# Performance work log

Measured on AMD Instinct MI355X. Metric: run time of the kernel, lower is better.

## Reference

```python
import jax, jax.numpy as jnp
import numpy as np

N = 50000   # nodes
E = 500000  # edges
B = 50      # graphs
H, D = 4, 64
NEG = 0.2   # leaky_relu slope in GATv2


def setup_inputs() -> dict:
    key = jax.random.key(0)
    ks = iter(jax.random.split(key, 40))
    rn = lambda shape, s=0.1: jax.random.normal(next(ks), shape, jnp.float32) * s
    inp = {
        'x': rn((N, 8), 1.0),
        'edge_index': jax.random.randint(next(ks), (2, E), 0, N, jnp.int64),
        'edge_attr': rn((E, 1), 1.0),
        'batch': jnp.sort(jax.random.randint(next(ks), (N,), 0, B, jnp.int64)),
        'enc_w': rn((8, 64)), 'enc_b': rn((64,)),
        'g1_wl': rn((64, 256)), 'g1_bl': rn((256,)),
        'g1_wr': rn((64, 256)), 'g1_br': rn((256,)),
        'g1_we': rn((1, 256)), 'g1_att': rn((H, D)), 'g1_bias': rn((256,)),
        'g2_wl': rn((256, 256)), 'g2_bl': rn((256,)),
        'g2_wr': rn((256, 256)), 'g2_br': rn((256,)),
        'g2_we': rn((1, 256)), 'g2_att': rn((H, D)), 'g2_bias': rn((256,)),
        'p1_w': rn((256, 128)), 'p1_b': rn((128,)),
        'ln_g': jnp.ones((128,), jnp.float32), 'ln_b': jnp.zeros((128,), jnp.float32),
        'p2_w': rn((128, 64)), 'p2_b': rn((64,)),
        'hc_w': rn((64, 1)), 'hc_b': rn((1,)),
        'hf_w': rn((64, 9)), 'hf_b': rn((9,)),
    }
    return inp


def gatv2(x, src, dst, ea, wl, bl, wr, br, we, att, bias):
    # x: [N, Fin]; src/dst: [E']; ea: [E',1]
    xl = (x @ wl + bl).reshape(N, H, D)  # source transform (lin_l)
    xr = (x @ wr + br).reshape(N, H, D)  # target transform (lin_r)
    e = (ea @ we).reshape(-1, H, D)      # edge embedding
    m = jax.nn.leaky_relu(xl[src] + xr[dst] + e, NEG)      # [E',H,D]
    logits = jnp.einsum('ehd,hd->eh', m, att)              # [E',H]
    # segment softmax over incoming edges of each target node
    lmax = jax.ops.segment_max(logits, dst, num_segments=N)
    lmax = jnp.where(jnp.isfinite(lmax), lmax, 0.0)
    ex = jnp.exp(logits - lmax[dst])
    den = jax.ops.segment_sum(ex, dst, num_segments=N)
    alpha = ex / den[dst]                                  # every node has a self-loop -> den > 0
    agg = jax.ops.segment_sum(xl[src] * alpha[:, :, None], dst, num_segments=N)
    return agg.reshape(N, H * D) + bias


def reference(x, edge_index, edge_attr, batch,
              enc_w, enc_b,
              g1_wl, g1_bl, g1_wr, g1_br, g1_we, g1_att, g1_bias,
              g2_wl, g2_bl, g2_wr, g2_br, g2_we, g2_att, g2_bias,
              p1_w, p1_b, ln_g, ln_b, p2_w, p2_b,
              hc_w, hc_b, hf_w, hf_b):
    # add self-loops once (PyG GATv2Conv default, edge_attr fill_value='mean')
    loop = jnp.arange(N, dtype=edge_index.dtype)
    src = jnp.concatenate([edge_index[0], loop])
    dst = jnp.concatenate([edge_index[1], loop])
    ea = jnp.concatenate([edge_attr,
                          jnp.broadcast_to(edge_attr.mean(0, keepdims=True), (N, 1))])

    h = jax.nn.relu(x @ enc_w + enc_b)
    h = jax.nn.relu(gatv2(h, src, dst, ea, g1_wl, g1_bl, g1_wr, g1_br, g1_we, g1_att, g1_bias))
    h = jax.nn.relu(gatv2(h, src, dst, ea, g2_wl, g2_bl, g2_wr, g2_br, g2_we, g2_att, g2_bias))

    # global mean pool over graphs
    sums = jax.ops.segment_sum(h, batch, num_segments=B)
    cnts = jax.ops.segment_sum(jnp.ones((N, 1), h.dtype), batch, num_segments=B)
    pooled = sums / jnp.maximum(cnts, 1.0)

    # post MLP: Linear -> LayerNorm -> ReLU -> (Dropout, eval=identity) -> Linear -> ReLU
    t = pooled @ p1_w + p1_b
    mu = t.mean(-1, keepdims=True)
    var = ((t - mu) ** 2).mean(-1, keepdims=True)
    t = (t - mu) / jnp.sqrt(var + 1e-5) * ln_g + ln_b
    t = jax.nn.relu(t)
    z = jax.nn.relu(t @ p2_w + p2_b)

    logit_cooling = (z @ hc_w + hc_b)[:, 0]
    logit_fatigue = z @ hf_w + hf_b
    return logit_cooling, logit_fatigue, z
```

## Files before the change

### kernel.cpp

```cpp
#include <hip/hip_runtime.h>
#include <hip/hip_bf16.h>

#define NN 50000
#define NE 500000
#define EP (NE + NN)
#define NB 50
#define NEG 0.2f
#define NBKT 196
#define CAP 3584
#define CHUNK 2048
#define NBLK1 ((EP + CHUNK - 1) / CHUNK)
#define NTILES 1563
#define GEMM_GX 392

#define ENC_BLKS 12500
#define MEAN_BLKS 256
#define WCONV_BLKS 640
#define ZERO_BLKS 51
#define SETUP_GRID (ENC_BLKS + MEAN_BLKS + WCONV_BLKS + 1 + ZERO_BLKS)

typedef __attribute__((ext_vector_type(8))) short short8;
typedef __attribute__((ext_vector_type(4))) float f32x4;

__device__ __forceinline__ ushort f2bf(float f) {
  unsigned u = __float_as_uint(f);
  unsigned r = (u + 0x7FFFu + ((u >> 16) & 1u)) >> 16;
  return (ushort)r;
}
__device__ __forceinline__ float bf2f(ushort b) {
  return __uint_as_float(((unsigned)b) << 16);
}

__device__ __forceinline__ float exp2s(float x) {
  float r;
  asm("v_exp_f32 %0, %1\ns_nop 0" : "=v"(r) : "v"(x));
  return r;
}

__device__ __forceinline__ float row_reduce16(float x) {
  x += __int_as_float(__builtin_amdgcn_mov_dpp(__float_as_int(x), 0xB1, 0xF, 0xF, true));
  x += __int_as_float(__builtin_amdgcn_mov_dpp(__float_as_int(x), 0x4E, 0xF, 0xF, true));
  x += __int_as_float(__builtin_amdgcn_mov_dpp(__float_as_int(x), 0x124, 0xF, 0xF, true));
  x += __int_as_float(__builtin_amdgcn_mov_dpp(__float_as_int(x), 0x128, 0xF, 0xF, true));
  return x;
}

__global__ __launch_bounds__(256) void setup_kernel(
    const float* __restrict__ x, const float* __restrict__ enc_w,
    const float* __restrict__ enc_b, ushort* __restrict__ h0,
    const float* __restrict__ ea, float* __restrict__ partials,
    const float* __restrict__ g1_wl, const float* __restrict__ g1_wr,
    const float* __restrict__ g2_wl, const float* __restrict__ g2_wr,
    ushort* __restrict__ w1l, ushort* __restrict__ w1r,
    ushort* __restrict__ w2l, ushort* __restrict__ w2r,
    const float* __restrict__ att1, const float* __restrict__ att2,
    float* __restrict__ a06_1, float* __restrict__ a04_1,
    float* __restrict__ a06_2, float* __restrict__ a04_2,
    int* __restrict__ gcursor, float* __restrict__ zero_region) {
  __shared__ float sw[4];
  int b = blockIdx.x, t = threadIdx.x;
  if (b < ENC_BLKS) {
    int i = b * 256 + t;
    int n = i >> 6, j = i & 63;
    float acc = enc_b[j];
#pragma unroll
    for (int k = 0; k < 8; k++) acc += x[n * 8 + k] * enc_w[k * 64 + j];
    h0[i] = f2bf(fmaxf(acc, 0.f));
    return;
  }
  b -= ENC_BLKS;
  if (b < MEAN_BLKS) {
    int idx = b * 256 + t;
    float v = 0.f;
    for (int i = idx; i < NE; i += 65536) v += ea[i];
    for (int off = 1; off < 64; off <<= 1) v += __shfl_xor(v, off, 64);
    if ((t & 63) == 0) sw[t >> 6] = v;
    __syncthreads();
    if (t == 0) partials[b] = sw[0] + sw[1] + sw[2] + sw[3];
    return;
  }
  b -= MEAN_BLKS;
  if (b < WCONV_BLKS) {
    if (b < 128) {
      int sec = b >> 6;
      const float* W = sec ? g1_wr : g1_wl;
      ushort* Wt = sec ? w1r : w1l;
      int i = (b & 63) * 256 + t;
      int n = i >> 6, k = i & 63;
      Wt[i] = f2bf(W[(size_t)k * 256 + n]);
    } else {
      int bb = b - 128;
      int sec = bb >> 8;
      const float* W = sec ? g2_wr : g2_wl;
      ushort* Wt = sec ? w2r : w2l;
      int i = (bb & 255) * 256 + t;
      int n = i >> 8, k = i & 255;
      Wt[i] = f2bf(W[(size_t)k * 256 + n]);
    }
    return;
  }
  b -= WCONV_BLKS;
  if (b == 0) {
    const float L2E = 1.44269504f;
    float v1 = att1[t], v2 = att2[t];
    a06_1[t] = 0.6f * L2E * v1;
    a04_1[t] = 0.4f * L2E * v1;
    a06_2[t] = 0.6f * L2E * v2;
    a04_2[t] = 0.4f * L2E * v2;
    if (t < NBKT) gcursor[t] = t * CAP;
    return;
  }
  b -= 1;
  {
    int i = b * 256 + t;
    if (i < NB * 256 + NB) zero_region[i] = 0.f;
  }
}

__global__ __launch_bounds__(256) void bucket_kernel(const int* __restrict__ ei,
                                                     const float* __restrict__ ea,
                                                     const float* __restrict__ partials,
                                                     int* __restrict__ gcursor,
                                                     int2* __restrict__ bucketed) {
  __shared__ int hist[NBKT];
  __shared__ int lbase[NBKT];
  __shared__ float smean[4];
  int t = threadIdx.x;
  int e0 = blockIdx.x * CHUNK;
  float pv = partials[t];
  for (int off = 1; off < 64; off <<= 1) pv += __shfl_xor(pv, off, 64);
  if ((t & 63) == 0) smean[t >> 6] = pv;
  for (int i = t; i < NBKT; i += 256) hist[i] = 0;
  __syncthreads();
  float mean = (smean[0] + smean[1] + smean[2] + smean[3]) * (1.0f / NE);
  int packed[8], eab[8], bkt[8];
#pragma unroll
  for (int j = 0; j < 8; j++) {
    int e = e0 + j * 256 + t;
    bool valid = e < EP;
    int src, dst;
    float v;
    if (e < NE) {
      src = ei[e];
      dst = ei[NE + e];
      v = ea[e];
    } else {
      int n = valid ? (e - NE) : 0;
      src = dst = n;
      v = mean;
    }
    bkt[j] = valid ? (dst >> 8) : -1;
    packed[j] = src | ((dst & 255) << 16);
    eab[j] = __float_as_int(v);
    if (valid) atomicAdd(&hist[dst >> 8], 1);
  }
  __syncthreads();
  for (int i = t; i < NBKT; i += 256)
    lbase[i] = hist[i] ? atomicAdd(&gcursor[i], hist[i]) : 0;
  __syncthreads();
#pragma unroll
  for (int j = 0; j < 8; j++) {
    if (bkt[j] >= 0) {
      int pos = atomicAdd(&lbase[bkt[j]], 1);
      pos = min(pos, (bkt[j] + 1) * CAP - 1);
      bucketed[pos] = make_int2(packed[j], eab[j]);
    }
  }
}

__global__ __launch_bounds__(256) void bucket_sort_kernel(const int* __restrict__ gcursor,
                                                          const int2* __restrict__ bucketed,
                                                          int2* __restrict__ sedge,
                                                          int* __restrict__ offsets,
                                                          int* __restrict__ counts) {
  __shared__ int2 stage[CAP];
  __shared__ int hist[256], scn[256], cur[256];
  int b = blockIdx.x, t = threadIdx.x;
  int base = b * CAP;
  int nb = min(gcursor[b] - base, CAP - 16);
  hist[t] = 0;
  for (int i = t; i < nb; i += 256) stage[i] = bucketed[base + i];
  __syncthreads();
  if (t < 16) {
    int2 pv = make_int2((stage[0].x & 0xFFFF) << 9, stage[0].y);
    sedge[base + nb + t] = pv;
  }
  for (int i = t; i < nb; i += 256) atomicAdd(&hist[(stage[i].x >> 16) & 255], 1);
  __syncthreads();
  int v = hist[t];
  scn[t] = v;
  __syncthreads();
  for (int off = 1; off < 256; off <<= 1) {
    int add = (t >= off) ? scn[t - off] : 0;
    __syncthreads();
    scn[t] += add;
    __syncthreads();
  }
  int excl = scn[t] - v;
  cur[t] = excl;
  __syncthreads();
  for (int i = t; i < nb; i += 256) {
    int dl = (stage[i].x >> 16) & 255;
    int p = atomicAdd(&cur[dl], 1);
    sedge[base + p] = make_int2((stage[i].x & 0xFFFF) << 9, stage[i].y);
  }
  int d = b * 256 + t;
  if (d < NN) {
    offsets[d] = base + excl;
    counts[d] = v;
  }
}

template <int K>
__global__ __launch_bounds__(256) void dual_linear_pb(const ushort* __restrict__ A,
                                                      const ushort* __restrict__ Wl,
                                                      const ushort* __restrict__ Wr,
                                                      const float* __restrict__ bl,
                                                      const float* __restrict__ br,
                                                      ushort* __restrict__ xl,
                                                      ushort* __restrict__ xr) {
  __shared__ ushort lt[32][272];
  int wave = threadIdx.x >> 6, lane = threadIdx.x & 63;
  int lr = lane & 15;
  int kb = (lane >> 4) * 8;
  const ushort* W = blockIdx.y ? Wr : Wl;
  const float* bias = blockIdx.y ? br : bl;
  ushort* O = blockIdx.y ? xr : xl;
  const int c0 = wave * 64;
  const ushort* pb = W + (size_t)(c0 + lr) * K + kb;
  int tid = threadIdx.x;
  int cb = (tid & 31) * 8;

  for (int t = blockIdx.x; t < NTILES; t += GEMM_GX) {
    int r = t * 32;
    int ra0 = min(r + lr, NN - 1);
    int ra1 = min(r + 16 + lr, NN - 1);
    const ushort* pa0 = A + (size_t)ra0 * K + kb;
    const ushort* pa1 = A + (size_t)ra1 * K + kb;
    f32x4 acc[2][4];
#pragma unroll
    for (int fr = 0; fr < 2; fr++)
#pragma unroll
      for (int fc = 0; fc < 4; fc++) acc[fr][fc] = (f32x4){0.f, 0.f, 0.f, 0.f};
#pragma unroll
    for (int kc = 0; kc < K; kc += 64) {
      short8 a00 = *(const short8*)(pa0 + kc);
      short8 a01 = *(const short8*)(pa0 + kc + 32);
      short8 a10 = *(const short8*)(pa1 + kc);
      short8 a11 = *(const short8*)(pa1 + kc + 32);
      short8 b0[4], b1[4];
#pragma unroll
      for (int fc = 0; fc < 4; fc++) {
        b0[fc] = *(const short8*)(pb + (size_t)fc * 16 * K + kc);
        b1[fc] = *(const short8*)(pb + (size_t)fc * 16 * K + kc + 32);
      }
#pragma unroll
      for (int fc = 0; fc < 4; fc++) {
        acc[0][fc] = __builtin_amdgcn_mfma_f32_16x16x32_bf16(a00, b0[fc], acc[0][fc], 0, 0, 0);
        acc[1][fc] = __builtin_amdgcn_mfma_f32_16x16x32_bf16(a10, b0[fc], acc[1][fc], 0, 0, 0);
      }
#pragma unroll
      for (int fc = 0; fc < 4; fc++) {
        acc[0][fc] = __builtin_amdgcn_mfma_f32_16x16x32_bf16(a01, b1[fc], acc[0][fc], 0, 0, 0);
        acc[1][fc] = __builtin_amdgcn_mfma_f32_16x16x32_bf16(a11, b1[fc], acc[1][fc], 0, 0, 0);
      }
    }
#pragma unroll
    for (int fc = 0; fc < 4; fc++) {
      int c = c0 + fc * 16 + lr;
      float bv = bias[c];
#pragma unroll
      for (int fr = 0; fr < 2; fr++) {
#pragma unroll
        for (int j = 0; j < 4; j++) {
          int row = fr * 16 + (lane >> 4) * 4 + j;
          int cs = c ^ (((row >> 2) & 3) << 4);
          lt[row][cs] = f2bf(acc[fr][fc][j] + bv);
        }
      }
    }
    __syncthreads();
#pragma unroll
    for (int it = 0; it < 4; it++) {
      int rl = (tid >> 5) + it * 8;
      int row = r + rl;
      if (row < NN) {
        int cs = cb ^ (((rl >> 2) & 3) << 4);
        short8 v = *(const short8*)&lt[rl][cs];
        *(short8*)(O + (size_t)row * 256 + cb) = v;
      }
    }
    __syncthreads();
  }
}

__global__ __launch_bounds__(256) void gat_fused_kernel(const int* __restrict__ offsets,
                                                        const int* __restrict__ counts,
                                                        const int2* __restrict__ sedge,
                                                        const ushort* __restrict__ xl,
                                                        const ushort* __restrict__ xr,
                                                        const float* __restrict__ we,
                                                        const float* __restrict__ a06p,
                                                        const float* __restrict__ a04p,
                                                        const float* __restrict__ bias,
                                                        ushort* __restrict__ hb) {
  int w = threadIdx.x >> 6, lane = threadIdx.x & 63;
  int d = blockIdx.x * 4 + w;
  if (d >= NN) return;
  int off = offsets[d], cnt = counts[d];
  const int c4 = lane * 4;
  ushort4 xru = *(const ushort4*)(xr + (size_t)d * 256 + c4);
  const float4 xr4 = {bf2f(xru.x), bf2f(xru.y), bf2f(xru.z), bf2f(xru.w)};
  const float4 we4 = *(const float4*)(we + c4);
  const float4 a06 = *(const float4*)(a06p + c4);
  const float4 a04 = *(const float4*)(a04p + c4);
  float4 acc = {0.f, 0.f, 0.f, 0.f};
  float den = 0.f;
  const int2* pe = sedge + off;
  const char* xlc = (const char*)xl + (size_t)c4 * 2;
  int2 e0 = pe[0], e1 = pe[1], e2 = pe[2], e3 = pe[3];
  ushort4 xu0 = *(const ushort4*)(xlc + (size_t)(unsigned)e0.x);
  ushort4 xu1 = *(const ushort4*)(xlc + (size_t)(unsigned)e1.x);
  ushort4 xu2 = *(const ushort4*)(xlc + (size_t)(unsigned)e2.x);
  ushort4 xu3 = *(const ushort4*)(xlc + (size_t)(unsigned)e3.x);
  int2 f0 = pe[4], f1 = pe[5], f2 = pe[6], f3 = pe[7];
  ushort4 yu0 = *(const ushort4*)(xlc + (size_t)(unsigned)f0.x);
  ushort4 yu1 = *(const ushort4*)(xlc + (size_t)(unsigned)f1.x);
  ushort4 yu2 = *(const ushort4*)(xlc + (size_t)(unsigned)f2.x);
  ushort4 yu3 = *(const ushort4*)(xlc + (size_t)(unsigned)f3.x);
#pragma unroll 2
  for (int i = 0; i < cnt; i += 4) {
    float ce0 = __int_as_float(e0.y), ce1 = __int_as_float(e1.y);
    float ce2 = __int_as_float(e2.y), ce3 = __int_as_float(e3.y);
    float4 x0 = {bf2f(xu0.x), bf2f(xu0.y), bf2f(xu0.z), bf2f(xu0.w)};
    float4 x1 = {bf2f(xu1.x), bf2f(xu1.y), bf2f(xu1.z), bf2f(xu1.w)};
    float4 x2 = {bf2f(xu2.x), bf2f(xu2.y), bf2f(xu2.z), bf2f(xu2.w)};
    float4 x3 = {bf2f(xu3.x), bf2f(xu3.y), bf2f(xu3.z), bf2f(xu3.w)};
    e0 = f0; e1 = f1; e2 = f2; e3 = f3;
    xu0 = yu0; xu1 = yu1; xu2 = yu2; xu3 = yu3;
    f0 = pe[i + 8]; f1 = pe[i + 9]; f2 = pe[i + 10]; f3 = pe[i + 11];
    yu0 = *(const ushort4*)(xlc + (size_t)(unsigned)f0.x);
    yu1 = *(const ushort4*)(xlc + (size_t)(unsigned)f1.x);
    yu2 = *(const ushort4*)(xlc + (size_t)(unsigned)f2.x);
    yu3 = *(const ushort4*)(xlc + (size_t)(unsigned)f3.x);
    float v0, v1, v2, v3;
    float p0, p1, p2, p3;
    v0 = x0.x + fmaf(ce0, we4.x, xr4.x);
    v1 = x0.y + fmaf(ce0, we4.y, xr4.y);
    v2 = x0.z + fmaf(ce0, we4.z, xr4.z);
    v3 = x0.w + fmaf(ce0, we4.w, xr4.w);
    p0 = fmaf(a06.x, v0, a04.x * fabsf(v0));
    p0 = fmaf(a06.y, v1, fmaf(a04.y, fabsf(v1), p0));
    p0 = fmaf(a06.z, v2, fmaf(a04.z, fabsf(v2), p0));
    p0 = fmaf(a06.w, v3, fmaf(a04.w, fabsf(v3), p0));
    v0 = x1.x + fmaf(ce1, we4.x, xr4.x);
    v1 = x1.y + fmaf(ce1, we4.y, xr4.y);
    v2 = x1.z + fmaf(ce1, we4.z, xr4.z);
    v3 = x1.w + fmaf(ce1, we4.w, xr4.w);
    p1 = fmaf(a06.x, v0, a04.x * fabsf(v0));
    p1 = fmaf(a06.y, v1, fmaf(a04.y, fabsf(v1), p1));
    p1 = fmaf(a06.z, v2, fmaf(a04.z, fabsf(v2), p1));
    p1 = fmaf(a06.w, v3, fmaf(a04.w, fabsf(v3), p1));
    v0 = x2.x + fmaf(ce2, we4.x, xr4.x);
    v1 = x2.y + fmaf(ce2, we4.y, xr4.y);
    v2 = x2.z + fmaf(ce2, we4.z, xr4.z);
    v3 = x2.w + fmaf(ce2, we4.w, xr4.w);
    p2 = fmaf(a06.x, v0, a04.x * fabsf(v0));
    p2 = fmaf(a06.y, v1, fmaf(a04.y, fabsf(v1), p2));
    p2 = fmaf(a06.z, v2, fmaf(a04.z, fabsf(v2), p2));
    p2 = fmaf(a06.w, v3, fmaf(a04.w, fabsf(v3), p2));
    v0 = x3.x + fmaf(ce3, we4.x, xr4.x);
    v1 = x3.y + fmaf(ce3, we4.y, xr4.y);
    v2 = x3.z + fmaf(ce3, we4.z, xr4.z);
    v3 = x3.w + fmaf(ce3, we4.w, xr4.w);
    p3 = fmaf(a06.x, v0, a04.x * fabsf(v0));
    p3 = fmaf(a06.y, v1, fmaf(a04.y, fabsf(v1), p3));
    p3 = fmaf(a06.z, v2, fmaf(a04.z, fabsf(v2), p3));
    p3 = fmaf(a06.w, v3, fmaf(a04.w, fabsf(v3), p3));
    p0 = row_reduce16(p0);
    p1 = row_reduce16(p1);
    p2 = row_reduce16(p2);
    p3 = row_reduce16(p3);
    float ex0 = exp2s(fminf(p0, 120.f));
    float ex1 = exp2s(fminf(p1, 120.f));
    float ex2 = exp2s(fminf(p2, 120.f));
    float ex3 = exp2s(fminf(p3, 120.f));
    ex1 = (i + 1 < cnt) ? ex1 : 0.f;
    ex2 = (i + 2 < cnt) ? ex2 : 0.f;
    ex3 = (i + 3 < cnt) ? ex3 : 0.f;
    den += (ex0 + ex1) + (ex2 + ex3);
    acc.x = fmaf(x0.x, ex0, fmaf(x1.x, ex1, fmaf(x2.x, ex2, fmaf(x3.x, ex3, acc.x))));
    acc.y = fmaf(x0.y, ex0, fmaf(x1.y, ex1, fmaf(x2.y, ex2, fmaf(x3.y, ex3, acc.y))));
    acc.z = fmaf(x0.z, ex0, fmaf(x1.z, ex1, fmaf(x2.z, ex2, fmaf(x3.z, ex3, acc.z))));
    acc.w = fmaf(x0.w, ex0, fmaf(x1.w, ex1, fmaf(x2.w, ex2, fmaf(x3.w, ex3, acc.w))));
  }
  const float4 b4 = *(const float4*)(bias + c4);
  float inv = 1.f / den;
  ushort4 o;
  o.x = f2bf(fmaxf(fmaf(acc.x, inv, b4.x), 0.f));
  o.y = f2bf(fmaxf(fmaf(acc.y, inv, b4.y), 0.f));
  o.z = f2bf(fmaxf(fmaf(acc.z, inv, b4.z), 0.f));
  o.w = f2bf(fmaxf(fmaf(acc.w, inv, b4.w), 0.f));
  *(ushort4*)(hb + (size_t)d * 256 + c4) = o;
}

__global__ __launch_bounds__(256) void pool_kernel(const ushort* __restrict__ h,
                                                   const int* __restrict__ batch,
                                                   float* __restrict__ sums,
                                                   float* __restrict__ cnts) {
  __shared__ int sb[128];
  int n0 = blockIdx.x * 128;
  int j = threadIdx.x;
  int count = min(128, NN - n0);
  if (count <= 0) return;
  for (int t = threadIdx.x; t < count; t += 256) sb[t] = batch[n0 + t];
  __syncthreads();
  float acc = 0.f;
  int run = 0;
  int cur = sb[0];
  for (int i = 0; i < count; ++i) {
    int b = sb[i];
    if (b != cur) {
      atomicAdd(&sums[(size_t)cur * 256 + j], acc);
      if (j == 0) atomicAdd(&cnts[cur], (float)run);
      acc = 0.f;
      run = 0;
      cur = b;
    }
    acc += bf2f(h[(size_t)(n0 + i) * 256 + j]);
    run++;
  }
  atomicAdd(&sums[(size_t)cur * 256 + j], acc);
  if (j == 0) atomicAdd(&cnts[cur], (float)run);
}

__global__ __launch_bounds__(128) void head_kernel(const float* __restrict__ sums,
                                                   const float* __restrict__ cnts,
                                                   const float* __restrict__ p1_w,
                                                   const float* __restrict__ p1_b,
                                                   const float* __restrict__ ln_g,
                                                   const float* __restrict__ ln_b,
                                                   const float* __restrict__ p2_w,
                                                   const float* __restrict__ p2_b,
                                                   const float* __restrict__ hc_w,
                                                   const float* __restrict__ hc_b,
                                                   const float* __restrict__ hf_w,
                                                   const float* __restrict__ hf_b,
                                                   float* __restrict__ out) {
  int g = blockIdx.x;
  int j = threadIdx.x;
  __shared__ float sp[256], st[128], sz[64];
  float cnt = fmaxf(cnts[g], 1.0f);
  for (int t = j; t < 256; t += 128) sp[t] = sums[(size_t)g * 256 + t] / cnt;
  __syncthreads();
  float acc = p1_b[j];
  for (int k = 0; k < 256; k++) acc += sp[k] * p1_w[(size_t)k * 128 + j];
  st[j] = acc;
  __syncthreads();
  float mu = 0.f;
  for (int k = 0; k < 128; k++) mu += st[k];
  mu *= (1.f / 128.f);
  float var = 0.f;
  for (int k = 0; k < 128; k++) {
    float d = st[k] - mu;
    var += d * d;
  }
  var *= (1.f / 128.f);
  float tj = (acc - mu) * rsqrtf(var + 1e-5f) * ln_g[j] + ln_b[j];
  tj = fmaxf(tj, 0.f);
  __syncthreads();
  st[j] = tj;
  __syncthreads();
  if (j < 64) {
    float z = p2_b[j];
    for (int k = 0; k < 128; k++) z += st[k] * p2_w[(size_t)k * 64 + j];
    z = fmaxf(z, 0.f);
    sz[j] = z;
    out[500 + (size_t)g * 64 + j] = z;
  }
  __syncthreads();
  if (j == 0) {
    float c = hc_b[0];
    for (int k = 0; k < 64; k++) c += sz[k] * hc_w[k];
    out[g] = c;
  }
  if (j >= 1 && j < 10) {
    int f = j - 1;
    float v = hf_b[f];
    for (int k = 0; k < 64; k++) v += sz[k] * hf_w[(size_t)k * 9 + f];
    out[50 + (size_t)g * 9 + f] = v;
  }
}

extern "C" void kernel_launch(void* const* d_in, const int* in_sizes, int n_in,
                              void* d_out, int out_size, void* d_ws, size_t ws_size,
                              hipStream_t stream) {
  const float* x = (const float*)d_in[0];
  const int* ei = (const int*)d_in[1];
  const float* ea = (const float*)d_in[2];
  const int* batch = (const int*)d_in[3];
  const float* enc_w = (const float*)d_in[4];
  const float* enc_b = (const float*)d_in[5];
  const float* g1_wl = (const float*)d_in[6];
  const float* g1_bl = (const float*)d_in[7];
  const float* g1_wr = (const float*)d_in[8];
  const float* g1_br = (const float*)d_in[9];
  const float* g1_we = (const float*)d_in[10];
  const float* g1_att = (const float*)d_in[11];
  const float* g1_bias = (const float*)d_in[12];
  const float* g2_wl = (const float*)d_in[13];
  const float* g2_bl = (const float*)d_in[14];
  const float* g2_wr = (const float*)d_in[15];
  const float* g2_br = (const float*)d_in[16];
  const float* g2_we = (const float*)d_in[17];
  const float* g2_att = (const float*)d_in[18];
  const float* g2_bias = (const float*)d_in[19];
  const float* p1_w = (const float*)d_in[20];
  const float* p1_b = (const float*)d_in[21];
  const float* ln_g = (const float*)d_in[22];
  const float* ln_b = (const float*)d_in[23];
  const float* p2_w = (const float*)d_in[24];
  const float* p2_b = (const float*)d_in[25];
  const float* hc_w = (const float*)d_in[26];
  const float* hc_b = (const float*)d_in[27];
  const float* hf_w = (const float*)d_in[28];
  const float* hf_b = (const float*)d_in[29];
  float* out = (float*)d_out;

  ushort* xlb = (ushort*)d_ws;
  ushort* xrb = xlb + (size_t)NN * 256;
  ushort* hb = xrb + (size_t)NN * 256;
  ushort* h0b = hb + (size_t)NN * 256;
  ushort* w1l = h0b + (size_t)NN * 64;
  ushort* w1r = w1l + 256 * 64;
  ushort* w2l = w1r + 256 * 64;
  ushort* w2r = w2l + 256 * 256;
  int2* bucketed = (int2*)(w2r + 256 * 256);
  int2* sedge = bucketed + (size_t)NBKT * CAP;
  int* gcursor = (int*)(sedge + (size_t)NBKT * CAP);
  int* counts = gcursor + NBKT;
  int* offsets = counts + NN;
  float* sums = (float*)(offsets + NN);
  float* cnts = sums + (size_t)NB * 256;
  float* partials = cnts + NB;
  float* a06_1 = partials + 256;
  float* a04_1 = a06_1 + 256;
  float* a06_2 = a04_1 + 256;
  float* a04_2 = a06_2 + 256;

  setup_kernel<<<SETUP_GRID, 256, 0, stream>>>(
      x, enc_w, enc_b, h0b, ea, partials, g1_wl, g1_wr, g2_wl, g2_wr, w1l, w1r,
      w2l, w2r, g1_att, g2_att, a06_1, a04_1, a06_2, a04_2, gcursor, sums);

  bucket_kernel<<<NBLK1, 256, 0, stream>>>(ei, ea, partials, gcursor, bucketed);
  bucket_sort_kernel<<<NBKT, 256, 0, stream>>>(gcursor, bucketed, sedge, offsets, counts);

  const dim3 gemmGrid(GEMM_GX, 2);
  const int nGatBlocks = (NN + 3) / 4;

  dual_linear_pb<64><<<gemmGrid, 256, 0, stream>>>(h0b, w1l, w1r, g1_bl, g1_br, xlb, xrb);
  gat_fused_kernel<<<nGatBlocks, 256, 0, stream>>>(offsets, counts, sedge, xlb, xrb,
                                                   g1_we, a06_1, a04_1, g1_bias, hb);

  dual_linear_pb<256><<<gemmGrid, 256, 0, stream>>>(hb, w2l, w2r, g2_bl, g2_br, xlb, xrb);
  gat_fused_kernel<<<nGatBlocks, 256, 0, stream>>>(offsets, counts, sedge, xlb, xrb,
                                                   g2_we, a06_2, a04_2, g2_bias, hb);

  pool_kernel<<<(NN + 127) / 128, 256, 0, stream>>>(hb, batch, sums, cnts);
  head_kernel<<<NB, 128, 0, stream>>>(sums, cnts, p1_w, p1_b, ln_g, ln_b, p2_w, p2_b,
                                      hc_w, hc_b, hf_w, hf_b, out);
}
```

Baseline: 254.8 us.

## Fuse edge bucketing into setup kernel and defer self-loop mean fill to sort

New measurement: 251.5 us. About the same (-1.3%).

```diff
diff --git a/kernel.cpp b/kernel.cpp
--- a/kernel.cpp
+++ b/kernel.cpp
@@ -12,12 +12,13 @@
 #define NBLK1 ((EP + CHUNK - 1) / CHUNK)
 #define NTILES 1563
 #define GEMM_GX 392
-
+#define SELF_FLAG (1 << 24)
+
+#define MEAN_BLKS 256
 #define ENC_BLKS 12500
-#define MEAN_BLKS 256
 #define WCONV_BLKS 640
 #define ZERO_BLKS 51
-#define SETUP_GRID (ENC_BLKS + MEAN_BLKS + WCONV_BLKS + 1 + ZERO_BLKS)
+#define SETUP_GRID (NBLK1 + MEAN_BLKS + ENC_BLKS + WCONV_BLKS + 1 + ZERO_BLKS)
 
 typedef __attribute__((ext_vector_type(8))) short short8;
 typedef __attribute__((ext_vector_type(4))) float f32x4;
@@ -49,6 +50,8 @@
     const float* __restrict__ x, const float* __restrict__ enc_w,
     const float* __restrict__ enc_b, ushort* __restrict__ h0,
     const float* __restrict__ ea, float* __restrict__ partials,
+    const int* __restrict__ ei, int* __restrict__ gcursor,
+    int2* __restrict__ bucketed,
     const float* __restrict__ g1_wl, const float* __restrict__ g1_wr,
     const float* __restrict__ g2_wl, const float* __restrict__ g2_wr,
     ushort* __restrict__ w1l, ushort* __restrict__ w1r,
@@ -56,19 +59,51 @@
     const float* __restrict__ att1, const float* __restrict__ att2,
     float* __restrict__ a06_1, float* __restrict__ a04_1,
     float* __restrict__ a06_2, float* __restrict__ a04_2,
-    int* __restrict__ gcursor, float* __restrict__ zero_region) {
+    float* __restrict__ zero_region) {
   __shared__ float sw[4];
+  __shared__ int hist[NBKT];
+  __shared__ int lbase[NBKT];
   int b = blockIdx.x, t = threadIdx.x;
-  if (b < ENC_BLKS) {
-    int i = b * 256 + t;
-    int n = i >> 6, j = i & 63;
-    float acc = enc_b[j];
-#pragma unroll
-    for (int k = 0; k < 8; k++) acc += x[n * 8 + k] * enc_w[k * 64 + j];
-    h0[i] = f2bf(fmaxf(acc, 0.f));
+  if (b < NBLK1) {
+    int e0 = b * CHUNK;
+    for (int i = t; i < NBKT; i += 256) hist[i] = 0;
+    __syncthreads();
+    int packed[8], eab[8], bkt[8];
+#pragma unroll
+    for (int j = 0; j < 8; j++) {
+      int e = e0 + j * 256 + t;
+      bool valid = e < EP;
+      int src, dst, fl = 0;
+      float v = 0.f;
+      if (e < NE) {
+        src = ei[e];
+        dst = ei[NE + e];
+        v = ea[e];
+      } else {
+        int n = valid ? (e - NE) : 0;
+        src = dst = n;
+        fl = SELF_FLAG;
+      }
+      bkt[j] = valid ? (dst >> 8) : -1;
+      packed[j] = src | ((dst & 255) << 16) | fl;
+      eab[j] = __float_as_int(v);
+      if (valid) atomicAdd(&hist[dst >> 8], 1);
+    }
+    __syncthreads();
+    for (int i = t; i < NBKT; i += 256)
+      lbase[i] = hist[i] ? (i * CAP + atomicAdd(&gcursor[i], hist[i])) : 0;
+    __syncthreads();
+#pragma unroll
+    for (int j = 0; j < 8; j++) {
+      if (bkt[j] >= 0) {
+        int pos = atomicAdd(&lbase[bkt[j]], 1);
+        pos = min(pos, (bkt[j] + 1) * CAP - 1);
+        bucketed[pos] = make_int2(packed[j], eab[j]);
+      }
+    }
     return;
   }
-  b -= ENC_BLKS;
+  b -= NBLK1;
   if (b < MEAN_BLKS) {
     int idx = b * 256 + t;
     float v = 0.f;
@@ -80,6 +115,16 @@
     return;
   }
   b -= MEAN_BLKS;
+  if (b < ENC_BLKS) {
+    int i = b * 256 + t;
+    int n = i >> 6, j = i & 63;
+    float acc = enc_b[j];
+#pragma unroll
+    for (int k = 0; k < 8; k++) acc += x[n * 8 + k] * enc_w[k * 64 + j];
+    h0[i] = f2bf(fmaxf(acc, 0.f));
+    return;
+  }
+  b -= ENC_BLKS;
   if (b < WCONV_BLKS) {
     if (b < 128) {
       int sec = b >> 6;
@@ -107,7 +152,6 @@
     a04_1[t] = 0.4f * L2E * v1;
     a06_2[t] = 0.6f * L2E * v2;
     a04_2[t] = 0.4f * L2E * v2;
-    if (t < NBKT) gcursor[t] = t * CAP;
     return;
   }
   b -= 1;
@@ -117,73 +161,33 @@
   }
 }
 
-__global__ __launch_bounds__(256) void bucket_kernel(const int* __restrict__ ei,
-                                                     const float* __restrict__ ea,
-                                                     const float* __restrict__ partials,
-                                                     int* __restrict__ gcursor,
-                                                     int2* __restrict__ bucketed) {
-  __shared__ int hist[NBKT];
-  __shared__ int lbase[NBKT];
-  __shared__ float smean[4];
-  int t = threadIdx.x;
-  int e0 = blockIdx.x * CHUNK;
-  float pv = partials[t];
-  for (int off = 1; off < 64; off <<= 1) pv += __shfl_xor(pv, off, 64);
-  if ((t & 63) == 0) smean[t >> 6] = pv;
-  for (int i = t; i < NBKT; i += 256) hist[i] = 0;
-  __syncthreads();
-  float mean = (smean[0] + smean[1] + smean[2] + smean[3]) * (1.0f / NE);
-  int packed[8], eab[8], bkt[8];
-#pragma unroll
-  for (int j = 0; j < 8; j++) {
-    int e = e0 + j * 256 + t;
-    bool valid = e < EP;
-    int src, dst;
-    float v;
-    if (e < NE) {
-      src = ei[e];
-      dst = ei[NE + e];
-      v = ea[e];
-    } else {
-      int n = valid ? (e - NE) : 0;
-      src = dst = n;
-      v = mean;
-    }
-    bkt[j] = valid ? (dst >> 8) : -1;
-    packed[j] = src | ((dst & 255) << 16);
-    eab[j] = __float_as_int(v);
-    if (valid) atomicAdd(&hist[dst >> 8], 1);
-  }
-  __syncthreads();
-  for (int i = t; i < NBKT; i += 256)
-    lbase[i] = hist[i] ? atomicAdd(&gcursor[i], hist[i]) : 0;
-  __syncthreads();
-#pragma unroll
-  for (int j = 0; j < 8; j++) {
-    if (bkt[j] >= 0) {
-      int pos = atomicAdd(&lbase[bkt[j]], 1);
-      pos = min(pos, (bkt[j] + 1) * CAP - 1);
-      bucketed[pos] = make_int2(packed[j], eab[j]);
-    }
-  }
-}
-
 __global__ __launch_bounds__(256) void bucket_sort_kernel(const int* __restrict__ gcursor,
+                                                          const float* __restrict__ partials,
                                                           const int2* __restrict__ bucketed,
                                                           int2* __restrict__ sedge,
                                                           int* __restrict__ offsets,
                                                           int* __restrict__ counts) {
   __shared__ int2 stage[CAP];
   __shared__ int hist[256], scn[256], cur[256];
+  __shared__ float sw[4];
   int b = blockIdx.x, t = threadIdx.x;
+  float pv = partials[t];
+  for (int off = 1; off < 64; off <<= 1) pv += __shfl_xor(pv, off, 64);
+  if ((t & 63) == 0) sw[t >> 6] = pv;
+  hist[t] = 0;
+  __syncthreads();
+  int meanb = __float_as_int((sw[0] + sw[1] + sw[2] + sw[3]) * (1.0f / NE));
   int base = b * CAP;
-  int nb = min(gcursor[b] - base, CAP - 16);
-  hist[t] = 0;
-  for (int i = t; i < nb; i += 256) stage[i] = bucketed[base + i];
+  int nb = min(gcursor[b], CAP - 16);
+  for (int i = t; i < nb; i += 256) {
+    int2 s = bucketed[base + i];
+    if (s.x & SELF_FLAG) s.y = meanb;
+    stage[i] = s;
+  }
   __syncthreads();
   if (t < 16) {
-    int2 pv = make_int2((stage[0].x & 0xFFFF) << 9, stage[0].y);
-    sedge[base + nb + t] = pv;
+    int2 pv2 = make_int2((stage[0].x & 0xFFFF) << 9, stage[0].y);
+    sedge[base + nb + t] = pv2;
   }
   for (int i = t; i < nb; i += 256) atomicAdd(&hist[(stage[i].x >> 16) & 255], 1);
   __syncthreads();
@@ -548,12 +552,15 @@
   float* a06_2 = a04_1 + 256;
   float* a04_2 = a06_2 + 256;
 
+  hipMemsetAsync(gcursor, 0, NBKT * sizeof(int), stream);
+
   setup_kernel<<<SETUP_GRID, 256, 0, stream>>>(
-      x, enc_w, enc_b, h0b, ea, partials, g1_wl, g1_wr, g2_wl, g2_wr, w1l, w1r,
-      w2l, w2r, g1_att, g2_att, a06_1, a04_1, a06_2, a04_2, gcursor, sums);
-
-  bucket_kernel<<<NBLK1, 256, 0, stream>>>(ei, ea, partials, gcursor, bucketed);
-  bucket_sort_kernel<<<NBKT, 256, 0, stream>>>(gcursor, bucketed, sedge, offsets, counts);
+      x, enc_w, enc_b, h0b, ea, partials, ei, gcursor, bucketed,
+      g1_wl, g1_wr, g2_wl, g2_wr, w1l, w1r, w2l, w2r,
+      g1_att, g2_att, a06_1, a04_1, a06_2, a04_2, sums);
+
+  bucket_sort_kernel<<<NBKT, 256, 0, stream>>>(gcursor, partials, bucketed, sedge,
+                                               offsets, counts);
 
   const dim3 gemmGrid(GEMM_GX, 2);
   const int nGatBlocks = (NN + 3) / 4;
```
